# Performance work log

Hardware: AMD Instinct MI355X
Metric: run time of the kernel (lower is better)

Reference implementation:

```python
import jax, jax.numpy as jnp
import numpy as np

EPS = 1e-8  # torch F.cosine_similarity default eps


def setup_inputs() -> dict:
    key = jax.random.key(0)
    k1, k2, k3, k4 = jax.random.split(key, 4)
    U, I, L = 8192, 8192, 256
    # xavier_uniform bound for Embedding weight (fan_in=n, fan_out=L)
    bu = float(np.sqrt(6.0 / (U + L)))
    bi = float(np.sqrt(6.0 / (I + L)))
    user_embed_w = jax.random.uniform(k1, (U, L), jnp.float32, -bu, bu)
    item_embed_w = jax.random.uniform(k2, (I, L), jnp.float32, -bi, bi)
    user_idx = jax.random.randint(k3, (1024,), 0, U, dtype=jnp.int64 if jax.config.jax_enable_x64 else jnp.int32)
    item_idx = jax.random.randint(k4, (1024,), 0, I, dtype=jnp.int64 if jax.config.jax_enable_x64 else jnp.int32)
    return {
        "user_embed_w": user_embed_w,
        "item_embed_w": item_embed_w,
        "user_idx": user_idx,
        "item_idx": item_idx,
        "is_test": 1,
    }


def _cosine_full(u, v):
    # Faithful to F.cosine_similarity(u[:,None], v[None,:], dim=-1) but
    # expressed as normalize + GEMM: (u.v) / (max(|u|,eps)*max(|v|,eps)).
    un = u / jnp.maximum(jnp.linalg.norm(u, axis=-1, keepdims=True), EPS)
    vn = v / jnp.maximum(jnp.linalg.norm(v, axis=-1, keepdims=True), EPS)
    return jnp.einsum("ul,il->ui", un, vn)  # [U, I]


def reference(user_embed_w, item_embed_w, user_idx, item_idx, is_test):
    if is_test:
        return _cosine_full(user_embed_w, item_embed_w)
    # training path: per-pair cosine similarity of user embeddings (note:
    # original code looks up BOTH indices in user_embed, faithfully kept)
    a = user_embed_w[user_idx]
    b = user_embed_w[item_idx]
    num = jnp.sum(a * b, axis=-1)
    den = jnp.maximum(jnp.linalg.norm(a, axis=-1), EPS) * jnp.maximum(
        jnp.linalg.norm(b, axis=-1), EPS
    )
    return (num / den).reshape(-1, 1)
```

## Files before the change

### kernel.cpp

```cpp
#include <hip/hip_runtime.h>
#include <hip/hip_bf16.h>
#include <stdint.h>


#define LDIM 256
#define NROWS 8192
#define NDIM 8192

typedef __bf16 bf16x8 __attribute__((ext_vector_type(8)));
typedef float f32x4 __attribute__((ext_vector_type(4)));

__device__ __forceinline__ unsigned short f2bf_rne(float f) {
  union { float f; uint32_t u; } c;
  c.f = f;
  uint32_t u = c.u;
  u += 0x7FFFu + ((u >> 16) & 1u);
  return (unsigned short)(u >> 16);
}

__global__ __launch_bounds__(256) void normalize_bf16(
    const float* __restrict__ src, unsigned short* __restrict__ dst) {
  const int wave = threadIdx.x >> 6;
  const int lane = threadIdx.x & 63;
  const int row = blockIdx.x * 4 + wave;

  const float4 v = reinterpret_cast<const float4*>(src + (size_t)row * LDIM)[lane];
  float ss = v.x * v.x + v.y * v.y + v.z * v.z + v.w * v.w;
#pragma unroll
  for (int off = 32; off; off >>= 1) ss += __shfl_xor(ss, off, 64);
  const float rn = 1.0f / fmaxf(sqrtf(ss), 1e-8f);

  ushort4 o;
  o.x = f2bf_rne(v.x * rn);
  o.y = f2bf_rne(v.y * rn);
  o.z = f2bf_rne(v.z * rn);
  o.w = f2bf_rne(v.w * rn);
  reinterpret_cast<ushort4*>(dst + (size_t)row * LDIM)[lane] = o;
}

#define BM 128
#define BN 128
#define BK 32

__device__ __forceinline__ void gld_lds16(const __bf16* g, __bf16* l) {
  __builtin_amdgcn_global_load_lds(
      (const __attribute__((address_space(1))) uint32_t*)g,
      (__attribute__((address_space(3))) uint32_t*)l, 16, 0, 0);
}

__global__ __launch_bounds__(256) void cos_gemm(
    const __bf16* __restrict__ A, const __bf16* __restrict__ B,
    float* __restrict__ C) {
  __shared__ __bf16 As[BM][BK];
  __shared__ __bf16 Bs[BN][BK];

  const int tid  = threadIdx.x;
  const int wid  = tid >> 6;
  const int lane = tid & 63;
  const int bn = blockIdx.x;
  const int bm = blockIdx.y;
  const int wr = wid >> 1;
  const int wc = wid & 1;

  const int m0 = (wid << 5) + (lane >> 2);
  const int k0 = (lane & 3) << 3;

  const __bf16* gA = A + (size_t)(bm * BM + m0) * LDIM + k0;
  const __bf16* gB = B + (size_t)(bn * BN + m0) * LDIM + k0;
  __bf16* lA = &As[0][0] + (wid << 10);
  __bf16* lB = &Bs[0][0] + (wid << 10);

  const int fr = lane & 15;
  const int kq = (lane >> 4) << 3;

  f32x4 acc[4][4] = {};

  for (int kt = 0; kt < LDIM / BK; ++kt) {
    const int ko = kt * BK;
#pragma unroll
    for (int c = 0; c < 2; ++c) {
      gld_lds16(gA + (size_t)(c * 16) * LDIM + ko, lA + (c << 9));
      gld_lds16(gB + (size_t)(c * 16) * LDIM + ko, lB + (c << 9));
    }
    __syncthreads();

    bf16x8 af[4], bfr[4];
#pragma unroll
    for (int m = 0; m < 4; ++m)
      af[m] = *reinterpret_cast<const bf16x8*>(&As[wr * 64 + m * 16 + fr][kq]);
#pragma unroll
    for (int n = 0; n < 4; ++n)
      bfr[n] = *reinterpret_cast<const bf16x8*>(&Bs[wc * 64 + n * 16 + fr][kq]);

#pragma unroll
    for (int m = 0; m < 4; ++m)
#pragma unroll
      for (int n = 0; n < 4; ++n)
        acc[m][n] = __builtin_amdgcn_mfma_f32_16x16x32_bf16(af[m], bfr[n],
                                                            acc[m][n], 0, 0, 0);
    __syncthreads();
  }

  const int r0 = (lane >> 4) << 2;
  float* Cp = C + (size_t)(bm * BM + wr * 64) * NDIM + (bn * BN + wc * 64);
#pragma unroll
  for (int m = 0; m < 4; ++m) {
#pragma unroll
    for (int n = 0; n < 4; ++n) {
      const f32x4 v = acc[m][n];
#pragma unroll
      for (int j = 0; j < 4; ++j)
        Cp[(size_t)(m * 16 + r0 + j) * NDIM + n * 16 + fr] = v[j];
    }
  }
}

extern "C" void kernel_launch(void* const* d_in, const int* in_sizes, int n_in,
                              void* d_out, int out_size, void* d_ws, size_t ws_size,
                              hipStream_t stream) {
  const float* user_w = (const float*)d_in[0];
  const float* item_w = (const float*)d_in[1];
  float* out = (float*)d_out;

  unsigned short* un = (unsigned short*)d_ws;
  unsigned short* vn = un + (size_t)NROWS * LDIM;

  normalize_bf16<<<NROWS / 4, 256, 0, stream>>>(user_w, un);
  normalize_bf16<<<NROWS / 4, 256, 0, stream>>>(item_w, vn);

  dim3 grid(NDIM / BN, NDIM / BM);
  cos_gemm<<<grid, 256, 0, stream>>>((const __bf16*)un, (const __bf16*)vn, out);
}
```

Measured before the change: 78.02 us.

## Double-buffer GEMM with BK=64, swizzled LDS, vector stores, fused normalize

Merges the two normalize launches into one kernel that covers both tables. The GEMM now uses BK=64 with double-buffered LDS, so the next tile loads while the current one computes. It also XOR-swizzles the LDS layout to avoid bank conflicts and swaps the MFMA operand order, so each lane writes contiguous 16-byte f32x4 output stores. This cuts launch overhead, sync count and store transactions in the output-write-bound GEMM, at the cost of more LDS per block (64KB), which may lower occupancy.

```diff
diff --git a/kernel.cpp b/kernel.cpp
--- a/kernel.cpp
+++ b/kernel.cpp
@@ -6,6 +6,9 @@
 #define LDIM 256
 #define NROWS 8192
 #define NDIM 8192
+#define BM 128
+#define BN 128
+#define BK 64
 
 typedef __bf16 bf16x8 __attribute__((ext_vector_type(8)));
 typedef float f32x4 __attribute__((ext_vector_type(4)));
@@ -18,13 +21,17 @@
   return (unsigned short)(u >> 16);
 }
 
-__global__ __launch_bounds__(256) void normalize_bf16(
-    const float* __restrict__ src, unsigned short* __restrict__ dst) {
+__global__ __launch_bounds__(256) void normalize_both(
+    const float* __restrict__ userw, const float* __restrict__ itemw,
+    unsigned short* __restrict__ dst) {
   const int wave = threadIdx.x >> 6;
   const int lane = threadIdx.x & 63;
   const int row = blockIdx.x * 4 + wave;
+  const float* src = (row < NROWS)
+                         ? userw + (size_t)row * LDIM
+                         : itemw + (size_t)(row - NROWS) * LDIM;
 
-  const float4 v = reinterpret_cast<const float4*>(src + (size_t)row * LDIM)[lane];
+  const float4 v = reinterpret_cast<const float4*>(src)[lane];
   float ss = v.x * v.x + v.y * v.y + v.z * v.z + v.w * v.w;
 #pragma unroll
   for (int off = 32; off; off >>= 1) ss += __shfl_xor(ss, off, 64);
@@ -38,10 +45,6 @@
   reinterpret_cast<ushort4*>(dst + (size_t)row * LDIM)[lane] = o;
 }
 
-#define BM 128
-#define BN 128
-#define BK 32
-
 __device__ __forceinline__ void gld_lds16(const __bf16* g, __bf16* l) {
   __builtin_amdgcn_global_load_lds(
       (const __attribute__((address_space(1))) uint32_t*)g,
@@ -51,68 +54,74 @@
 __global__ __launch_bounds__(256) void cos_gemm(
     const __bf16* __restrict__ A, const __bf16* __restrict__ B,
     float* __restrict__ C) {
-  __shared__ __bf16 As[BM][BK];
-  __shared__ __bf16 Bs[BN][BK];
+  __shared__ __align__(16) __bf16 As[2][BM * BK];
+  __shared__ __align__(16) __bf16 Bs[2][BN * BK];
 
-  const int tid  = threadIdx.x;
-  const int wid  = tid >> 6;
+  const int tid = threadIdx.x;
+  const int wid = tid >> 6;
   const int lane = tid & 63;
-  const int bn = blockIdx.x;
-  const int bm = blockIdx.y;
-  const int wr = wid >> 1;
-  const int wc = wid & 1;
+  const int bn = blockIdx.x, bm = blockIdx.y;
+  const int wr = wid >> 1, wc = wid & 1;
 
-  const int m0 = (wid << 5) + (lane >> 2);
-  const int k0 = (lane & 3) << 3;
-
-  const __bf16* gA = A + (size_t)(bm * BM + m0) * LDIM + k0;
-  const __bf16* gB = B + (size_t)(bn * BN + m0) * LDIM + k0;
-  __bf16* lA = &As[0][0] + (wid << 10);
-  __bf16* lB = &Bs[0][0] + (wid << 10);
+  const int srow = tid >> 3;
+  const int scbx = (((tid & 7) ^ (srow & 7)) << 4);
+  const __bf16* gA = A + (size_t)(bm * BM + srow) * LDIM + (scbx >> 1);
+  const __bf16* gB = B + (size_t)(bn * BN + srow) * LDIM + (scbx >> 1);
 
   const int fr = lane & 15;
-  const int kq = (lane >> 4) << 3;
+  const int q = lane >> 4;
+  const int rsw = (fr & 7) << 4;
 
   f32x4 acc[4][4] = {};
 
-  for (int kt = 0; kt < LDIM / BK; ++kt) {
-    const int ko = kt * BK;
+#define STAGE(buf, kt)                                                       \
+  {                                                                          \
+    _Pragma("unroll") for (int c = 0; c < 4; ++c) {                          \
+      gld_lds16(gA + (size_t)(c * 32) * LDIM + (kt)*BK,                      \
+                &As[buf][c * 2048 + wid * 512]);                             \
+      gld_lds16(gB + (size_t)(c * 32) * LDIM + (kt)*BK,                      \
+                &Bs[buf][c * 2048 + wid * 512]);                             \
+    }                                                                        \
+  }
+
+#define COMPUTE(buf)                                                         \
+  {                                                                          \
+    _Pragma("unroll") for (int ks = 0; ks < 2; ++ks) {                       \
+      bf16x8 af[4], bv[4];                                                   \
+      const int kb = ((((ks << 6) | (q << 4)) ^ rsw) >> 1);                  \
+      _Pragma("unroll") for (int m = 0; m < 4; ++m)                          \
+          af[m] = *reinterpret_cast<const bf16x8*>(                          \
+              &As[buf][(wr * 64 + m * 16 + fr) * BK + kb]);                  \
+      _Pragma("unroll") for (int n = 0; n < 4; ++n)                          \
+          bv[n] = *reinterpret_cast<const bf16x8*>(                          \
+              &Bs[buf][(wc * 64 + n * 16 + fr) * BK + kb]);                  \
+      _Pragma("unroll") for (int m = 0; m < 4; ++m)                          \
+          _Pragma("unroll") for (int n = 0; n < 4; ++n)                      \
+              acc[m][n] = __builtin_amdgcn_mfma_f32_16x16x32_bf16(           \
+                  bv[n], af[m], acc[m][n], 0, 0, 0);                         \
+    }                                                                        \
+  }
+
+  STAGE(0, 0);
+  __syncthreads();
 #pragma unroll
-    for (int c = 0; c < 2; ++c) {
-      gld_lds16(gA + (size_t)(c * 16) * LDIM + ko, lA + (c << 9));
-      gld_lds16(gB + (size_t)(c * 16) * LDIM + ko, lB + (c << 9));
-    }
+  for (int kt = 0; kt < 3; ++kt) {
+    STAGE((kt + 1) & 1, kt + 1);
+    COMPUTE(kt & 1);
     __syncthreads();
+  }
+  COMPUTE(1);
 
-    bf16x8 af[4], bfr[4];
+  float* Cp = C + (size_t)(bm * BM + wr * 64 + fr) * NDIM +
+              (bn * BN + wc * 64 + (q << 2));
 #pragma unroll
-    for (int m = 0; m < 4; ++m)
-      af[m] = *reinterpret_cast<const bf16x8*>(&As[wr * 64 + m * 16 + fr][kq]);
+  for (int m = 0; m < 4; ++m)
 #pragma unroll
     for (int n = 0; n < 4; ++n)
-      bfr[n] = *reinterpret_cast<const bf16x8*>(&Bs[wc * 64 + n * 16 + fr][kq]);
-
-#pragma unroll
-    for (int m = 0; m < 4; ++m)
-#pragma unroll
-      for (int n = 0; n < 4; ++n)
-        acc[m][n] = __builtin_amdgcn_mfma_f32_16x16x32_bf16(af[m], bfr[n],
-                                                            acc[m][n], 0, 0, 0);
-    __syncthreads();
-  }
-
-  const int r0 = (lane >> 4) << 2;
-  float* Cp = C + (size_t)(bm * BM + wr * 64) * NDIM + (bn * BN + wc * 64);
-#pragma unroll
-  for (int m = 0; m < 4; ++m) {
-#pragma unroll
-    for (int n = 0; n < 4; ++n) {
-      const f32x4 v = acc[m][n];
-#pragma unroll
-      for (int j = 0; j < 4; ++j)
-        Cp[(size_t)(m * 16 + r0 + j) * NDIM + n * 16 + fr] = v[j];
-    }
-  }
+      *reinterpret_cast<f32x4*>(Cp + (size_t)(m * 16) * NDIM + n * 16) =
+          acc[m][n];
+#undef STAGE
+#undef COMPUTE
 }
 
 extern "C" void kernel_launch(void* const* d_in, const int* in_sizes, int n_in,
@@ -125,8 +134,7 @@
   unsigned short* un = (unsigned short*)d_ws;
   unsigned short* vn = un + (size_t)NROWS * LDIM;
 
-  normalize_bf16<<<NROWS / 4, 256, 0, stream>>>(user_w, un);
-  normalize_bf16<<<NROWS / 4, 256, 0, stream>>>(item_w, vn);
+  normalize_both<<<(2 * NROWS) / 4, 256, 0, stream>>>(user_w, item_w, un);
 
   dim3 grid(NDIM / BN, NDIM / BM);
   cos_gemm<<<grid, 256, 0, stream>>>((const __bf16*)un, (const __bf16*)vn, out);
```

Measured after the change: 82.88 us. 1.06x slower.
